# Kernel tuning notes

Hardware: AMD Instinct MI355X
Metric: run time of the kernel (lower is better)

The kernel has to match this reference:

```python
import jax, jax.numpy as jnp
import numpy as np

B, T, D_MODEL, D_HIDDEN = 4, 8192, 1024, 1024
EPS = 1e-5

def setup_inputs() -> dict:
    key = jax.random.key(0)
    ks = jax.random.split(key, 8)
    s_in = 1.0 / np.sqrt(D_MODEL)
    s_h = 1.0 / np.sqrt(D_HIDDEN)
    return {
        "x": jax.random.normal(ks[0], (B, T, D_MODEL), jnp.float32),
        "W_ih": jax.random.uniform(ks[1], (D_MODEL, D_HIDDEN), jnp.float32, -s_in, s_in),
        "b_ih": jnp.zeros((D_HIDDEN,), jnp.float32),
        "W_gate": jax.random.uniform(ks[2], (D_MODEL, D_HIDDEN), jnp.float32, -s_in, s_in),
        "b_gate": jnp.zeros((D_HIDDEN,), jnp.float32),
        "log_a": jnp.full((D_HIDDEN,), -0.1, jnp.float32),
        "ln_g": jnp.ones((D_HIDDEN,), jnp.float32),
        "ln_b": jnp.zeros((D_HIDDEN,), jnp.float32),
        "W_out": jax.random.uniform(ks[3], (D_HIDDEN, D_HIDDEN), jnp.float32, -s_h, s_h),
        "b_out": jnp.zeros((D_HIDDEN,), jnp.float32),
        "W_proj": jax.random.uniform(ks[4], (D_HIDDEN, D_MODEL), jnp.float32, -s_h, s_h),
        "b_proj": jnp.zeros((D_MODEL,), jnp.float32),
    }

def _scan(alpha, beta):
    # h_t = alpha_t * h_{t-1} + beta_t, h_0 = 0, over axis 1 (time)
    def combine(c1, c2):
        a1, b1 = c1
        a2, b2 = c2
        return a2 * a1, a2 * b1 + b2
    _, h = jax.lax.associative_scan(combine, (alpha, beta), axis=1)
    return h

def reference(x, W_ih, b_ih, W_gate, b_gate, log_a, ln_g, ln_b, W_out, b_out, W_proj, b_proj):
    ih = jnp.einsum("btd,dh->bth", x, W_ih) + b_ih
    gate = jax.nn.sigmoid(jnp.einsum("btd,dh->bth", x, W_gate) + b_gate)
    a = jnp.exp(log_a)  # [H]
    alpha = (1.0 - gate) * a  # [B,T,H]
    beta = gate * ih
    h = _scan(alpha, beta)
    # LayerNorm over last dim
    mu = jnp.mean(h, axis=-1, keepdims=True)
    var = jnp.var(h, axis=-1, keepdims=True)
    hn = (h - mu) * jax.lax.rsqrt(var + EPS) * ln_g + ln_b
    out = jnp.einsum("bth,ho->bto", hn, W_out) + b_out
    return jnp.einsum("bth,hd->btd", out, W_proj) + b_proj
```

## Files before the change

kernel.cpp:

```cpp
#include <hip/hip_runtime.h>

typedef short bhalf8 __attribute__((ext_vector_type(8)));
typedef float floatx4 __attribute__((ext_vector_type(4)));
typedef unsigned short ushortx8 __attribute__((ext_vector_type(8)));

__device__ __forceinline__ unsigned short f2bf(float f){
  union { float f; unsigned int u; } v; v.f = f;
  unsigned int u = v.u;
  u += 0x7fffu + ((u >> 16) & 1u);
  return (unsigned short)(u >> 16);
}
__device__ __forceinline__ float bf2f(unsigned short u){
  union { unsigned int u; float f; } v; v.u = ((unsigned)u) << 16; return v.f;
}
__device__ __forceinline__ unsigned pack2(float a, float b){
  return (unsigned)f2bf(a) | ((unsigned)f2bf(b) << 16);
}

__device__ __forceinline__ void async16(const unsigned short* g, unsigned short* l){
  __builtin_amdgcn_global_load_lds(
      (const __attribute__((address_space(1))) void*)g,
      (__attribute__((address_space(3))) void*)l,
      16, 0, 0);
}

template<int EPI>
__global__ __launch_bounds__(256) void gemm_k(
    const unsigned short* __restrict__ Ab, const unsigned short* __restrict__ BT,
    const float* __restrict__ bias, float* __restrict__ Cf,
    unsigned short* __restrict__ Cb, int K, int ldc)
{
  __shared__ __align__(16) unsigned short As[128*64];
  __shared__ __align__(16) unsigned short Bs[128*64];
  const int tid = threadIdx.x;
  const int n0 = blockIdx.x * 128;
  const int m0 = blockIdx.y * 128;
  const int wid = tid >> 6, lane = tid & 63;
  const int wr = (wid >> 1) * 64, wc = (wid & 1) * 64;
  const int r16 = lane & 15, quad = lane >> 4;
  const int ldsbase = (tid & ~63) * 8;

  const unsigned short* pA[4];
  const unsigned short* pB[4];
  #pragma unroll
  for (int i = 0; i < 4; ++i) {
    int p = tid + i*256;
    int row = p >> 3;
    int cp = (p & 7) ^ (row & 7);
    pA[i] = Ab + (size_t)(m0+row)*K + cp*8;
    pB[i] = BT + (size_t)(n0+row)*K + cp*8;
  }
  int aoff[2][4], boff[2][4];
  #pragma unroll
  for (int ks = 0; ks < 2; ++ks){
    #pragma unroll
    for (int mi = 0; mi < 4; ++mi){
      int row = wr + mi*16 + r16;
      aoff[ks][mi] = (row*8 + ((ks*4+quad) ^ (row&7))) * 8;
    }
    #pragma unroll
    for (int ni = 0; ni < 4; ++ni){
      int row = wc + ni*16 + r16;
      boff[ks][ni] = (row*8 + ((ks*4+quad) ^ (row&7))) * 8;
    }
  }

  floatx4 acc[4][4];
  #pragma unroll
  for (int i=0;i<4;i++)
    #pragma unroll
    for (int j2=0;j2<4;j2++) acc[i][j2] = {0.f,0.f,0.f,0.f};

  for (int k0 = 0; k0 < K; k0 += 64) {
    #pragma unroll
    for (int i = 0; i < 4; ++i) async16(pA[i], &As[ldsbase + i*2048]);
    #pragma unroll
    for (int i = 0; i < 4; ++i) async16(pB[i], &Bs[ldsbase + i*2048]);
    __syncthreads();
    #pragma unroll
    for (int ks = 0; ks < 2; ++ks) {
      bhalf8 aF[4], bF[4];
      #pragma unroll
      for (int mi=0;mi<4;++mi) aF[mi] = *(const bhalf8*)&As[aoff[ks][mi]];
      #pragma unroll
      for (int ni=0;ni<4;++ni) bF[ni] = *(const bhalf8*)&Bs[boff[ks][ni]];
      #pragma unroll
      for (int mi=0;mi<4;++mi)
        #pragma unroll
        for (int ni=0;ni<4;++ni)
          acc[mi][ni] = __builtin_amdgcn_mfma_f32_16x16x32_bf16(aF[mi], bF[ni], acc[mi][ni], 0, 0, 0);
    }
    __syncthreads();
    #pragma unroll
    for (int i = 0; i < 4; ++i) { pA[i] += 64; pB[i] += 64; }
  }

  #pragma unroll
  for (int mi=0;mi<4;++mi)
    #pragma unroll
    for (int ni=0;ni<4;++ni)
      #pragma unroll
      for (int rr=0;rr<4;++rr){
        int m = m0 + wr + mi*16 + quad*4 + rr;
        int n = n0 + wc + ni*16 + r16;
        float val = acc[mi][ni][rr];
        if (EPI == 0) Cf[(size_t)m*ldc + n] = val;
        else if (EPI == 1) Cf[(size_t)m*ldc + n] = val + bias[n];
        else if (EPI == 3) Cb[(size_t)m*ldc + n] = f2bf(val + bias[n]);
        else Cb[(size_t)n*ldc + m] = f2bf(val);
      }
}

__global__ __launch_bounds__(256) void prep_all(
    const float* __restrict__ W_ih, const float* __restrict__ W_gate,
    const float* __restrict__ W_proj, const float* __restrict__ W_out,
    const float* __restrict__ b_out,
    const float* __restrict__ log_a, const float* __restrict__ b_ih,
    const float* __restrict__ b_gate, const float* __restrict__ x,
    unsigned short* __restrict__ WcatT, unsigned short* __restrict__ WprojT,
    unsigned short* __restrict__ Woutb, unsigned short* __restrict__ xb,
    float* __restrict__ Pc, float* __restrict__ a_vec, float* __restrict__ bcat)
{
  __shared__ float tile[32][33];
  const int blk = blockIdx.x;
  const int tid = threadIdx.x;
  if (blk < 3072) {
    const int which = blk >> 10;
    const int t = blk & 1023;
    const float* src = (which == 0) ? W_ih : (which == 1) ? W_gate : W_proj;
    unsigned short* dst = (which == 0) ? WcatT : (which == 1) ? (WcatT + 1024*1024) : WprojT;
    const int c0 = (t & 31) * 32, r0 = (t >> 5) * 32;
    const int tx = tid & 31, ty = tid >> 5;
    #pragma unroll
    for (int i = 0; i < 32; i += 8)
      tile[ty+i][tx] = src[(size_t)(r0+ty+i)*1024 + c0+tx];
    __syncthreads();
    #pragma unroll
    for (int i = 0; i < 32; i += 8)
      dst[(size_t)(c0+ty+i)*1024 + r0+tx] = f2bf(tile[tx][ty+i]);
  } else if (blk < 4096) {
    int idx = ((blk - 3072)*256 + tid) * 4;
    float4 v = *(const float4*)(W_out + idx);
    uint2 p;
    p.x = pack2(v.x, v.y);
    p.y = pack2(v.z, v.w);
    *(uint2*)(Woutb + idx) = p;
  } else if (blk < 4160) {
    int blk2 = blk - 4096;
    int dgrp = blk2 >> 4, seg = blk2 & 15;
    int d = dgrp*256 + tid;
    int e0 = seg*64;
    float acc = 0.f;
    #pragma unroll 8
    for (int e = 0; e < 64; ++e)
      acc += b_out[e0+e] * W_proj[(size_t)(e0+e)*1024 + d];
    Pc[seg*1024 + d] = acc;
  } else if (blk < 4168) {
    int d = (blk - 4160)*256 + tid;
    if (d < 1024) {
      a_vec[d] = __expf(log_a[d]);
      bcat[d] = b_ih[d];
    } else {
      bcat[d] = b_gate[d-1024];
    }
  } else {
    int idx = ((blk - 4168)*256 + tid) * 4;
    float4 v = *(const float4*)(x + idx);
    uint2 p;
    p.x = pack2(v.x, v.y);
    p.y = pack2(v.z, v.w);
    *(uint2*)(xb + idx) = p;
  }
}

#define CHUNK 16
#define NCHUNK 512

__device__ __forceinline__ void ab_step(unsigned short iu, unsigned short gu,
                                        float a, float& al, float& be)
{
  float zi = bf2f(iu), zg = bf2f(gu);
  float g = __builtin_amdgcn_rcpf(1.f + __expf(-zg));
  al = (1.f - g) * a;
  be = g * zi;
}

__global__ __launch_bounds__(256, 4) void scan_phase1(const unsigned short* __restrict__ pre,
    const float* __restrict__ a_vec, float* __restrict__ AsT, float* __restrict__ SsT)
{
  __shared__ float sA[4][1024];
  __shared__ float sS[4][1024];
  int wid = threadIdx.x >> 6, lane = threadIdx.x & 63;
  int u = blockIdx.x*4 + wid;
  int b = u >> 9, c = u & (NCHUNK-1);
  int ch0 = lane*16;
  float a[16], A[16], S[16];
  #pragma unroll
  for (int q=0;q<4;++q) *(float4*)&a[q*4] = *(const float4*)(a_vec + ch0 + q*4);
  #pragma unroll
  for (int j=0;j<16;++j){ A[j]=1.f; S[j]=0.f; }
  size_t base = ((size_t)(b*8192 + c*CHUNK))*2048 + ch0;
  for (int t=0;t<CHUNK;++t){
    ushortx8 i0 = *(const ushortx8*)(pre + base);
    ushortx8 i1 = *(const ushortx8*)(pre + base + 8);
    ushortx8 g0 = *(const ushortx8*)(pre + base + 1024);
    ushortx8 g1 = *(const ushortx8*)(pre + base + 1032);
    #pragma unroll
    for (int j=0;j<8;++j){
      float al, be;
      ab_step(i0[j], g0[j], a[j], al, be);
      A[j] *= al; S[j] = al*S[j] + be;
      ab_step(i1[j], g1[j], a[j+8], al, be);
      A[j+8] *= al; S[j+8] = al*S[j+8] + be;
    }
    base += 2048;
  }
  #pragma unroll
  for (int j=0;j<16;++j){ sA[wid][ch0+j] = A[j]; sS[wid][ch0+j] = S[j]; }
  __syncthreads();
  const int bb = blockIdx.x >> 7;
  const int c0 = (blockIdx.x*4) & (NCHUNK-1);
  const int t = threadIdx.x;
  #pragma unroll
  for (int q=0;q<4;++q){
    int ch = t + q*256;
    float4 va = make_float4(sA[0][ch], sA[1][ch], sA[2][ch], sA[3][ch]);
    float4 vs = make_float4(sS[0][ch], sS[1][ch], sS[2][ch], sS[3][ch]);
    size_t o = ((size_t)(bb*1024 + ch))*NCHUNK + c0;
    *(float4*)(AsT + o) = va;
    *(float4*)(SsT + o) = vs;
  }
}

__global__ __launch_bounds__(256) void scan_phase2(const float* __restrict__ AsT,
    const float* __restrict__ SsT, float* __restrict__ carry,
    const float* __restrict__ Pc, const float* __restrict__ b_proj,
    float* __restrict__ b_comb)
{
  int wid = threadIdx.x >> 6, lane = threadIdx.x & 63;
  int p = blockIdx.x*4 + wid;
  size_t base = (size_t)p*NCHUNK + lane*8;
  float4 a0 = *(const float4*)(AsT + base);
  float4 a1 = *(const float4*)(AsT + base + 4);
  float4 s0 = *(const float4*)(SsT + base);
  float4 s1 = *(const float4*)(SsT + base + 4);
  float A = a0.x, S = s0.x;
  A = a0.y*A; S = a0.y*S + s0.y;
  A = a0.z*A; S = a0.z*S + s0.z;
  A = a0.w*A; S = a0.w*S + s0.w;
  A = a1.x*A; S = a1.x*S + s1.x;
  A = a1.y*A; S = a1.y*S + s1.y;
  A = a1.z*A; S = a1.z*S + s1.z;
  A = a1.w*A; S = a1.w*S + s1.w;
  float iA = A, iS = S;
  #pragma unroll
  for (int d = 1; d < 64; d <<= 1) {
    float pA = __shfl_up(iA, d);
    float pS = __shfl_up(iS, d);
    if (lane >= d) { iS = iA*pS + iS; iA = iA*pA; }
  }
  float bS = __shfl_up(iS, 1);
  if (lane == 0) bS = 0.f;
  const int b2 = p >> 10, ch = p & 1023;
  size_t o = ((size_t)b2*NCHUNK + lane*8)*1024 + ch;
  carry[o] = bS; bS = a0.x*bS + s0.x; o += 1024;
  carry[o] = bS; bS = a0.y*bS + s0.y; o += 1024;
  carry[o] = bS; bS = a0.z*bS + s0.z; o += 1024;
  carry[o] = bS; bS = a0.w*bS + s0.w; o += 1024;
  carry[o] = bS; bS = a1.x*bS + s1.x; o += 1024;
  carry[o] = bS; bS = a1.y*bS + s1.y; o += 1024;
  carry[o] = bS; bS = a1.z*bS + s1.z; o += 1024;
  carry[o] = bS;

  if (blockIdx.x == 0) {
    #pragma unroll
    for (int q = 0; q < 4; ++q) {
      int d = threadIdx.x + q*256;
      float acc = b_proj[d];
      #pragma unroll
      for (int s = 0; s < 16; ++s) acc += Pc[s*1024 + d];
      b_comb[d] = acc;
    }
  }
}

__global__ __launch_bounds__(256, 4) void scan_phase3(const unsigned short* __restrict__ pre,
    const float* __restrict__ a_vec, const float* __restrict__ carry,
    const float* __restrict__ ln_g, const float* __restrict__ ln_b,
    unsigned short* __restrict__ hn)
{
  int wid = threadIdx.x >> 6, lane = threadIdx.x & 63;
  int u = blockIdx.x*4 + wid;
  int b = u >> 9, c = u & (NCHUNK-1);
  int ch0 = lane*16;
  float a[16], h[16], g[16], lb[16];
  size_t co = ((size_t)b*NCHUNK + c)*1024 + ch0;
  #pragma unroll
  for (int q=0;q<4;++q){
    *(float4*)&a[q*4]  = *(const float4*)(a_vec + ch0 + q*4);
    *(float4*)&h[q*4]  = *(const float4*)(carry + co + q*4);
    *(float4*)&g[q*4]  = *(const float4*)(ln_g + ch0 + q*4);
    *(float4*)&lb[q*4] = *(const float4*)(ln_b + ch0 + q*4);
  }
  size_t base  = ((size_t)(b*8192 + c*CHUNK))*2048 + ch0;
  size_t hbase = ((size_t)(b*8192 + c*CHUNK))*1024 + ch0;
  for (int t=0;t<CHUNK;++t){
    ushortx8 i0 = *(const ushortx8*)(pre + base);
    ushortx8 i1 = *(const ushortx8*)(pre + base + 8);
    ushortx8 g0 = *(const ushortx8*)(pre + base + 1024);
    ushortx8 g1 = *(const ushortx8*)(pre + base + 1032);
    float s = 0.f, s2 = 0.f;
    #pragma unroll
    for (int j=0;j<8;++j){
      float al, be;
      ab_step(i0[j], g0[j], a[j], al, be);
      h[j] = al*h[j] + be;
      s += h[j]; s2 += h[j]*h[j];
      ab_step(i1[j], g1[j], a[j+8], al, be);
      h[j+8] = al*h[j+8] + be;
      s += h[j+8]; s2 += h[j+8]*h[j+8];
    }
    #pragma unroll
    for (int off = 32; off > 0; off >>= 1) {
      s  += __shfl_xor(s,  off);
      s2 += __shfl_xor(s2, off);
    }
    float mu = s * (1.f/1024.f);
    float var = s2 * (1.f/1024.f) - mu*mu;
    float rstd = __builtin_amdgcn_rsqf(var + 1e-5f);
    uint4 o0, o1;
    float v0, v1;
    v0 = (h[0]-mu)*rstd*g[0]+lb[0];  v1 = (h[1]-mu)*rstd*g[1]+lb[1];  o0.x = pack2(v0,v1);
    v0 = (h[2]-mu)*rstd*g[2]+lb[2];  v1 = (h[3]-mu)*rstd*g[3]+lb[3];  o0.y = pack2(v0,v1);
    v0 = (h[4]-mu)*rstd*g[4]+lb[4];  v1 = (h[5]-mu)*rstd*g[5]+lb[5];  o0.z = pack2(v0,v1);
    v0 = (h[6]-mu)*rstd*g[6]+lb[6];  v1 = (h[7]-mu)*rstd*g[7]+lb[7];  o0.w = pack2(v0,v1);
    v0 = (h[8]-mu)*rstd*g[8]+lb[8];  v1 = (h[9]-mu)*rstd*g[9]+lb[9];  o1.x = pack2(v0,v1);
    v0 = (h[10]-mu)*rstd*g[10]+lb[10]; v1 = (h[11]-mu)*rstd*g[11]+lb[11]; o1.y = pack2(v0,v1);
    v0 = (h[12]-mu)*rstd*g[12]+lb[12]; v1 = (h[13]-mu)*rstd*g[13]+lb[13]; o1.z = pack2(v0,v1);
    v0 = (h[14]-mu)*rstd*g[14]+lb[14]; v1 = (h[15]-mu)*rstd*g[15]+lb[15]; o1.w = pack2(v0,v1);
    *(uint4*)(hn + hbase)     = o0;
    *(uint4*)(hn + hbase + 8) = o1;
    base += 2048; hbase += 1024;
  }
}

extern "C" void kernel_launch(void* const* d_in, const int* in_sizes, int n_in,
                              void* d_out, int out_size, void* d_ws, size_t ws_size,
                              hipStream_t stream)
{
  const float* x      = (const float*)d_in[0];
  const float* W_ih   = (const float*)d_in[1];
  const float* b_ih   = (const float*)d_in[2];
  const float* W_gate = (const float*)d_in[3];
  const float* b_gate = (const float*)d_in[4];
  const float* log_a  = (const float*)d_in[5];
  const float* ln_g   = (const float*)d_in[6];
  const float* ln_b   = (const float*)d_in[7];
  const float* W_out  = (const float*)d_in[8];
  const float* b_out  = (const float*)d_in[9];
  const float* W_proj = (const float*)d_in[10];
  const float* b_proj = (const float*)d_in[11];
  float* out = (float*)d_out;

  char* ws = (char*)d_ws;
  size_t off = 0;
  auto alloc = [&](size_t bytes)->char* {
    char* p = ws + off; off += (bytes + 255) & ~(size_t)255; return p;
  };
  unsigned short* pre   = (unsigned short*)alloc((size_t)32768*2048*2);
  unsigned short* hn    = (unsigned short*)alloc((size_t)32768*1024*2);
  unsigned short* xb    = hn;
  unsigned short* WcatT = (unsigned short*)alloc((size_t)2048*1024*2);
  unsigned short* WprojT= (unsigned short*)alloc((size_t)1024*1024*2);
  unsigned short* Woutb = (unsigned short*)alloc((size_t)1024*1024*2);
  unsigned short* WcombT= (unsigned short*)alloc((size_t)1024*1024*2);
  float* AsT            = (float*)alloc((size_t)4*1024*NCHUNK*4);
  float* SsT            = (float*)alloc((size_t)4*1024*NCHUNK*4);
  float* carry          = (float*)alloc((size_t)4*NCHUNK*1024*4);
  float* Pc             = (float*)alloc((size_t)16*1024*4);
  float* b_comb         = (float*)alloc(1024*4);
  float* a_vec          = (float*)alloc(1024*4);
  float* bcat           = (float*)alloc(2048*4);

  prep_all<<<4168 + 32768, 256, 0, stream>>>(W_ih, W_gate, W_proj, W_out, b_out,
                                             log_a, b_ih, b_gate, x,
                                             WcatT, WprojT, Woutb, xb,
                                             Pc, a_vec, bcat);
  gemm_k<2><<<dim3(8,8), 256, 0, stream>>>(Woutb, WprojT, nullptr, nullptr, WcombT, 1024, 1024);
  gemm_k<3><<<dim3(16,256), 256, 0, stream>>>(xb, WcatT, bcat, nullptr, pre, 1024, 2048);
  scan_phase1<<<512, 256, 0, stream>>>(pre, a_vec, AsT, SsT);
  scan_phase2<<<1024, 256, 0, stream>>>(AsT, SsT, carry, Pc, b_proj, b_comb);
  scan_phase3<<<512, 256, 0, stream>>>(pre, a_vec, carry, ln_g, ln_b, hn);
  gemm_k<1><<<dim3(8,256), 256, 0, stream>>>(hn, WcombT, b_comb, out, nullptr, 1024, 1024);
}
```

Baseline: 615.7 us.

## Merge pre-activation and weight-combine GEMMs into one launch; halve scan chunk size

The two independent GEMMs (x·Wcat producing pre, and Wout·Wproj producing WcombT) now run in a single kernel launch with 4160 blocks, so the small weight GEMM fills gaps instead of running as a separate serialized launch. Separately, the scan chunk length drops from 16 to 8 timesteps, doubling the number of chunks and blocks in scan phases 1 and 3 for more parallelism. Phase 2 now handles 16 chunks per lane, and the AsT/SsT/carry buffers grow accordingly. The trade-offs are extra carry traffic and a longer serial section per lane in phase 2.

```diff
diff --git a/kernel.cpp b/kernel.cpp
--- a/kernel.cpp
+++ b/kernel.cpp
@@ -109,6 +109,107 @@
         else if (EPI == 3) Cb[(size_t)m*ldc + n] = f2bf(val + bias[n]);
         else Cb[(size_t)n*ldc + m] = f2bf(val);
       }
+}
+
+__global__ __launch_bounds__(256) void gemm_pre_wcomb(
+    const unsigned short* __restrict__ xb, const unsigned short* __restrict__ WcatT,
+    const float* __restrict__ bcat, unsigned short* __restrict__ pre,
+    const unsigned short* __restrict__ Woutb, const unsigned short* __restrict__ WprojT,
+    unsigned short* __restrict__ WcombT)
+{
+  __shared__ __align__(16) unsigned short As[128*64];
+  __shared__ __align__(16) unsigned short Bs[128*64];
+  const int blk = blockIdx.x;
+  const bool wjob = (blk >= 4096);
+  int n0, m0, ldc;
+  const unsigned short *Ab, *BT;
+  if (!wjob) { n0 = (blk & 15) * 128; m0 = (blk >> 4) * 128; Ab = xb;    BT = WcatT;  ldc = 2048; }
+  else { int t = blk - 4096; n0 = (t & 7) * 128; m0 = (t >> 3) * 128; Ab = Woutb; BT = WprojT; ldc = 1024; }
+  const int K = 1024;
+  const int tid = threadIdx.x;
+  const int wid = tid >> 6, lane = tid & 63;
+  const int wr = (wid >> 1) * 64, wc = (wid & 1) * 64;
+  const int r16 = lane & 15, quad = lane >> 4;
+  const int ldsbase = (tid & ~63) * 8;
+
+  const unsigned short* pA[4];
+  const unsigned short* pB[4];
+  #pragma unroll
+  for (int i = 0; i < 4; ++i) {
+    int p = tid + i*256;
+    int row = p >> 3;
+    int cp = (p & 7) ^ (row & 7);
+    pA[i] = Ab + (size_t)(m0+row)*K + cp*8;
+    pB[i] = BT + (size_t)(n0+row)*K + cp*8;
+  }
+  int aoff[2][4], boff[2][4];
+  #pragma unroll
+  for (int ks = 0; ks < 2; ++ks){
+    #pragma unroll
+    for (int mi = 0; mi < 4; ++mi){
+      int row = wr + mi*16 + r16;
+      aoff[ks][mi] = (row*8 + ((ks*4+quad) ^ (row&7))) * 8;
+    }
+    #pragma unroll
+    for (int ni = 0; ni < 4; ++ni){
+      int row = wc + ni*16 + r16;
+      boff[ks][ni] = (row*8 + ((ks*4+quad) ^ (row&7))) * 8;
+    }
+  }
+
+  floatx4 acc[4][4];
+  #pragma unroll
+  for (int i=0;i<4;i++)
+    #pragma unroll
+    for (int j2=0;j2<4;j2++) acc[i][j2] = {0.f,0.f,0.f,0.f};
+
+  for (int k0 = 0; k0 < K; k0 += 64) {
+    #pragma unroll
+    for (int i = 0; i < 4; ++i) async16(pA[i], &As[ldsbase + i*2048]);
+    #pragma unroll
+    for (int i = 0; i < 4; ++i) async16(pB[i], &Bs[ldsbase + i*2048]);
+    __syncthreads();
+    #pragma unroll
+    for (int ks = 0; ks < 2; ++ks) {
+      bhalf8 aF[4], bF[4];
+      #pragma unroll
+      for (int mi=0;mi<4;++mi) aF[mi] = *(const bhalf8*)&As[aoff[ks][mi]];
+      #pragma unroll
+      for (int ni=0;ni<4;++ni) bF[ni] = *(const bhalf8*)&Bs[boff[ks][ni]];
+      #pragma unroll
+      for (int mi=0;mi<4;++mi)
+        #pragma unroll
+        for (int ni=0;ni<4;++ni)
+          acc[mi][ni] = __builtin_amdgcn_mfma_f32_16x16x32_bf16(aF[mi], bF[ni], acc[mi][ni], 0, 0, 0);
+    }
+    __syncthreads();
+    #pragma unroll
+    for (int i = 0; i < 4; ++i) { pA[i] += 64; pB[i] += 64; }
+  }
+
+  if (!wjob) {
+    #pragma unroll
+    for (int mi=0;mi<4;++mi)
+      #pragma unroll
+      for (int ni=0;ni<4;++ni)
+        #pragma unroll
+        for (int rr=0;rr<4;++rr){
+          int m = m0 + wr + mi*16 + quad*4 + rr;
+          int n = n0 + wc + ni*16 + r16;
+          pre[(size_t)m*2048 + n] = f2bf(acc[mi][ni][rr] + bcat[n]);
+        }
+  } else {
+    #pragma unroll
+    for (int mi=0;mi<4;++mi)
+      #pragma unroll
+      for (int ni=0;ni<4;++ni)
+        #pragma unroll
+        for (int rr=0;rr<4;++rr){
+          int m = m0 + wr + mi*16 + quad*4 + rr;
+          int n = n0 + wc + ni*16 + r16;
+          WcombT[(size_t)n*1024 + m] = f2bf(acc[mi][ni][rr]);
+        }
+  }
 }
 
 __global__ __launch_bounds__(256) void prep_all(
@@ -173,8 +274,9 @@
   }
 }
 
-#define CHUNK 16
-#define NCHUNK 512
+#define CHUNK 8
+#define NCHUNK 1024
+#define CPL 16
 
 __device__ __forceinline__ void ab_step(unsigned short iu, unsigned short gu,
                                         float a, float& al, float& be)
@@ -192,7 +294,7 @@
   __shared__ float sS[4][1024];
   int wid = threadIdx.x >> 6, lane = threadIdx.x & 63;
   int u = blockIdx.x*4 + wid;
-  int b = u >> 9, c = u & (NCHUNK-1);
+  int b = u >> 10, c = u & (NCHUNK-1);
   int ch0 = lane*16;
   float a[16], A[16], S[16];
   #pragma unroll
@@ -218,7 +320,7 @@
   #pragma unroll
   for (int j=0;j<16;++j){ sA[wid][ch0+j] = A[j]; sS[wid][ch0+j] = S[j]; }
   __syncthreads();
-  const int bb = blockIdx.x >> 7;
+  const int bb = blockIdx.x >> 8;
   const int c0 = (blockIdx.x*4) & (NCHUNK-1);
   const int t = threadIdx.x;
   #pragma unroll
@@ -239,19 +341,16 @@
 {
   int wid = threadIdx.x >> 6, lane = threadIdx.x & 63;
   int p = blockIdx.x*4 + wid;
-  size_t base = (size_t)p*NCHUNK + lane*8;
-  float4 a0 = *(const float4*)(AsT + base);
-  float4 a1 = *(const float4*)(AsT + base + 4);
-  float4 s0 = *(const float4*)(SsT + base);
-  float4 s1 = *(const float4*)(SsT + base + 4);
-  float A = a0.x, S = s0.x;
-  A = a0.y*A; S = a0.y*S + s0.y;
-  A = a0.z*A; S = a0.z*S + s0.z;
-  A = a0.w*A; S = a0.w*S + s0.w;
-  A = a1.x*A; S = a1.x*S + s1.x;
-  A = a1.y*A; S = a1.y*S + s1.y;
-  A = a1.z*A; S = a1.z*S + s1.z;
-  A = a1.w*A; S = a1.w*S + s1.w;
+  size_t base = (size_t)p*NCHUNK + lane*CPL;
+  float av[CPL], sv[CPL];
+  #pragma unroll
+  for (int q=0;q<CPL/4;++q){
+    *(float4*)&av[q*4] = *(const float4*)(AsT + base + q*4);
+    *(float4*)&sv[q*4] = *(const float4*)(SsT + base + q*4);
+  }
+  float A = av[0], S = sv[0];
+  #pragma unroll
+  for (int j=1;j<CPL;++j){ S = av[j]*S + sv[j]; A = av[j]*A; }
   float iA = A, iS = S;
   #pragma unroll
   for (int d = 1; d < 64; d <<= 1) {
@@ -262,15 +361,13 @@
   float bS = __shfl_up(iS, 1);
   if (lane == 0) bS = 0.f;
   const int b2 = p >> 10, ch = p & 1023;
-  size_t o = ((size_t)b2*NCHUNK + lane*8)*1024 + ch;
-  carry[o] = bS; bS = a0.x*bS + s0.x; o += 1024;
-  carry[o] = bS; bS = a0.y*bS + s0.y; o += 1024;
-  carry[o] = bS; bS = a0.z*bS + s0.z; o += 1024;
-  carry[o] = bS; bS = a0.w*bS + s0.w; o += 1024;
-  carry[o] = bS; bS = a1.x*bS + s1.x; o += 1024;
-  carry[o] = bS; bS = a1.y*bS + s1.y; o += 1024;
-  carry[o] = bS; bS = a1.z*bS + s1.z; o += 1024;
-  carry[o] = bS;
+  size_t o = ((size_t)b2*NCHUNK + lane*CPL)*1024 + ch;
+  #pragma unroll
+  for (int j=0;j<CPL;++j){
+    carry[o] = bS;
+    bS = av[j]*bS + sv[j];
+    o += 1024;
+  }
 
   if (blockIdx.x == 0) {
     #pragma unroll
@@ -291,7 +388,7 @@
 {
   int wid = threadIdx.x >> 6, lane = threadIdx.x & 63;
   int u = blockIdx.x*4 + wid;
-  int b = u >> 9, c = u & (NCHUNK-1);
+  int b = u >> 10, c = u & (NCHUNK-1);
   int ch0 = lane*16;
   float a[16], h[16], g[16], lb[16];
   size_t co = ((size_t)b*NCHUNK + c)*1024 + ch0;
@@ -386,10 +483,10 @@
                                              log_a, b_ih, b_gate, x,
                                              WcatT, WprojT, Woutb, xb,
                                              Pc, a_vec, bcat);
-  gemm_k<2><<<dim3(8,8), 256, 0, stream>>>(Woutb, WprojT, nullptr, nullptr, WcombT, 1024, 1024);
-  gemm_k<3><<<dim3(16,256), 256, 0, stream>>>(xb, WcatT, bcat, nullptr, pre, 1024, 2048);
-  scan_phase1<<<512, 256, 0, stream>>>(pre, a_vec, AsT, SsT);
+  gemm_pre_wcomb<<<4160, 256, 0, stream>>>(xb, WcatT, bcat, pre,
+                                           Woutb, WprojT, WcombT);
+  scan_phase1<<<1024, 256, 0, stream>>>(pre, a_vec, AsT, SsT);
   scan_phase2<<<1024, 256, 0, stream>>>(AsT, SsT, carry, Pc, b_proj, b_comb);
-  scan_phase3<<<512, 256, 0, stream>>>(pre, a_vec, carry, ln_g, ln_b, hn);
+  scan_phase3<<<1024, 256, 0, stream>>>(pre, a_vec, carry, ln_g, ln_b, hn);
   gemm_k<1><<<dim3(8,256), 256, 0, stream>>>(hn, WcombT, b_comb, out, nullptr, 1024, 1024);
 }
```

New measurement: 774.8 us. +25.8%, slower.
